# Optimization experiments

Measured on AMD Instinct MI355X. Metric: run time of the kernel, lower is better.

The kernel has to match this reference:

```python
import jax, jax.numpy as jnp
import numpy as np

# pywt db2 decomposition filters
DEC_LO = np.array([-0.12940952255092145, 0.22414386804185735,
                   0.8365163037378079, 0.4829629131445341], dtype=np.float32)
DEC_HI = np.array([-0.4829629131445341, 0.8365163037378079,
                   -0.22414386804185735, -0.12940952255092145], dtype=np.float32)
LEVEL = 3
REC_WEIGHT = 1.0
FILT_LEN = 4
PAD = (2 * FILT_LEN - 3) // 2  # = 2, ptwt reflect padding per side


def _filters(dtype):
    # ptwt uses cross-correlation with flipped pywt filters (== true convolution)
    lo = jnp.asarray(DEC_LO[::-1].copy(), dtype=dtype)
    hi = jnp.asarray(DEC_HI[::-1].copy(), dtype=dtype)
    ll = jnp.outer(lo, lo)  # 'a'
    lh = jnp.outer(hi, lo)  # 'h'
    hl = jnp.outer(lo, hi)  # 'v'
    hh = jnp.outer(hi, hi)  # 'd'
    return jnp.stack([ll, lh, hl, hh])[:, None]  # [4,1,4,4]


def _dwt_step(x, filt):
    # x: [N, nb, H, W] -> [N, 4*nb, H', W'] (each band split into a,h,v,d; grouped)
    n, nb, h, w = x.shape
    padb = PAD + (h % 2)
    padr = PAD + (w % 2)
    xp = jnp.pad(x, ((0, 0), (0, 0), (PAD, padb), (PAD, padr)), mode='reflect')
    k = jnp.tile(filt, (nb, 1, 1, 1))  # [4*nb, 1, 4, 4]
    return jax.lax.conv_general_dilated(
        xp, k, window_strides=(2, 2), padding='VALID',
        feature_group_count=nb,
        dimension_numbers=('NCHW', 'OIHW', 'NCHW'))


def setup_inputs() -> dict:
    key = jax.random.key(0)
    k1, k2 = jax.random.split(key)
    preds = jax.random.normal(k1, (64, 3, 512, 512), dtype=jnp.float32)
    targets = jax.random.normal(k2, (64, 3, 512, 512), dtype=jnp.float32)
    return {"preds": preds, "targets": targets}


def reference(preds, targets):
    n, c, h, w = preds.shape
    p = preds.reshape(n * c, 1, h, w)
    t = targets.reshape(n * c, 1, h, w)
    filt = _filters(preds.dtype)
    for _ in range(LEVEL):
        p = _dwt_step(p, filt)
        t = _dwt_step(t, filt)
    # p, t: [N*C, 4**LEVEL, h', w']; leaf 0 is the all-'a' (pure approx) packet
    per_leaf_mse = jnp.mean((p - t) ** 2, axis=(0, 2, 3))  # [4**LEVEL]
    wvec = jnp.ones(per_leaf_mse.shape[0], dtype=preds.dtype).at[0].set(0.5)
    return REC_WEIGHT * jnp.dot(wvec, per_leaf_mse)
```

## Files before the change

kernel.cpp:

```cpp
#include <hip/hip_runtime.h>

#define F_LO0 0.4829629131445341f
#define F_LO1 0.8365163037378079f
#define F_LO2 0.22414386804185735f
#define F_LO3 (-0.12940952255092145f)
#define F_HI0 (-0.12940952255092145f)
#define F_HI1 (-0.22414386804185735f)
#define F_HI2 0.8365163037378079f
#define F_HI3 (-0.4829629131445341f)

__device__ __forceinline__ int reflect_idx(int r, int n) {
    r = (r < 0) ? -r : r;
    r = (r >= n) ? 2 * n - 2 - r : r;
    return r;
}

__device__ __forceinline__ float4 vfilt(const float4 a, const float4 b,
                                        const float4 c, const float4 d,
                                        float c0, float c1, float c2, float c3) {
    return make_float4(c0 * a.x + c1 * b.x + c2 * c.x + c3 * d.x,
                       c0 * a.y + c1 * b.y + c2 * c.y + c3 * d.y,
                       c0 * a.z + c1 * b.z + c2 * c.z + c3 * d.z,
                       c0 * a.w + c1 * b.w + c2 * c.w + c3 * d.w);
}

__global__ void __launch_bounds__(512) k_wpt_fused(
    const float* __restrict__ p, const float* __restrict__ t,
    float* __restrict__ partial) {
    constexpr int N0 = 512, N1 = 257, N2 = 130, N3 = 66;

    __shared__ __align__(16) float sA[6080];
    __shared__ __align__(16) float sB[6240];
    __shared__ float wsum[8];

    int bid = blockIdx.x;
    int swz = (bid & 7) * (int)(gridDim.x >> 3) + (bid >> 3);
    int img = swz / 81;
    int tt = swz - img * 81;
    int TA = (tt / 9) * 8;
    int TB = (tt % 9) * 8;

    const int tid = threadIdx.x;
    const size_t ibase = (size_t)img * (N0 * N0);

    const int O0r = 8 * TA - 14, O0c = 8 * TB - 16;
    const int O1r = 4 * TA - 6, O1c = 4 * TB - 6;
    const int O2r = 2 * TA - 2, O2c = 2 * TB - 2;
    const bool edge = (TA == 0) || (TA == 64) || (TB == 0) || (TB == 64);

    if (tid < 390) {
        unsigned ru = (unsigned)tid / 5u;
        const int r = (int)ru;
        const int k = tid - (int)(5u * ru);
        const int grr = reflect_idx(O0r + r, N0);
        const float* __restrict__ prow = p + ibase + (size_t)grr * N0;
        const float* __restrict__ trow = t + ibase + (size_t)grr * N0;
        const int gc0 = O0c + 16 * k;
        float v[20];
        if ((unsigned)gc0 <= 492u) {
#pragma unroll
            for (int q = 0; q < 5; ++q) {
                const float4 pv = *(const float4*)(prow + gc0 + 4 * q);
                const float4 tv = *(const float4*)(trow + gc0 + 4 * q);
                v[4 * q + 0] = pv.x - tv.x;
                v[4 * q + 1] = pv.y - tv.y;
                v[4 * q + 2] = pv.z - tv.z;
                v[4 * q + 3] = pv.w - tv.w;
            }
        } else {
#pragma unroll
            for (int x = 0; x < 20; ++x) {
                int gc = reflect_idx(gc0 + x, N0);
                v[x] = prow[gc] - trow[gc];
            }
        }
        float* dst = sB + r * 40 + 8 * k;
        *(float4*)(dst) = make_float4(
            F_LO0 * v[2] + F_LO1 * v[3] + F_LO2 * v[4] + F_LO3 * v[5],
            F_LO0 * v[4] + F_LO1 * v[5] + F_LO2 * v[6] + F_LO3 * v[7],
            F_LO0 * v[6] + F_LO1 * v[7] + F_LO2 * v[8] + F_LO3 * v[9],
            F_LO0 * v[8] + F_LO1 * v[9] + F_LO2 * v[10] + F_LO3 * v[11]);
        *(float4*)(dst + 4) = make_float4(
            F_LO0 * v[10] + F_LO1 * v[11] + F_LO2 * v[12] + F_LO3 * v[13],
            F_LO0 * v[12] + F_LO1 * v[13] + F_LO2 * v[14] + F_LO3 * v[15],
            F_LO0 * v[14] + F_LO1 * v[15] + F_LO2 * v[16] + F_LO3 * v[17],
            F_LO0 * v[16] + F_LO1 * v[17] + F_LO2 * v[18] + F_LO3 * v[19]);
        *(float4*)(dst + 3120) = make_float4(
            F_HI0 * v[2] + F_HI1 * v[3] + F_HI2 * v[4] + F_HI3 * v[5],
            F_HI0 * v[4] + F_HI1 * v[5] + F_HI2 * v[6] + F_HI3 * v[7],
            F_HI0 * v[6] + F_HI1 * v[7] + F_HI2 * v[8] + F_HI3 * v[9],
            F_HI0 * v[8] + F_HI1 * v[9] + F_HI2 * v[10] + F_HI3 * v[11]);
        *(float4*)(dst + 3124) = make_float4(
            F_HI0 * v[10] + F_HI1 * v[11] + F_HI2 * v[12] + F_HI3 * v[13],
            F_HI0 * v[12] + F_HI1 * v[13] + F_HI2 * v[14] + F_HI3 * v[15],
            F_HI0 * v[14] + F_HI1 * v[15] + F_HI2 * v[16] + F_HI3 * v[17],
            F_HI0 * v[16] + F_HI1 * v[17] + F_HI2 * v[18] + F_HI3 * v[19]);
    }
    __syncthreads();

    if (tid < 380) {
        int r1 = tid / 10, k = tid - (tid / 10) * 10;
        const float* blo = sB + (2 * r1) * 40 + 4 * k;
        const float* bhi = blo + 3120;
        float4 L0 = *(const float4*)(blo);
        float4 L1v = *(const float4*)(blo + 40);
        float4 L2v = *(const float4*)(blo + 80);
        float4 L3v = *(const float4*)(blo + 120);
        float4 H0 = *(const float4*)(bhi);
        float4 H1 = *(const float4*)(bhi + 40);
        float4 H2 = *(const float4*)(bhi + 80);
        float4 H3 = *(const float4*)(bhi + 120);
        float4 b0 = vfilt(L0, L1v, L2v, L3v, F_LO0, F_LO1, F_LO2, F_LO3);
        float4 b1 = vfilt(L0, L1v, L2v, L3v, F_HI0, F_HI1, F_HI2, F_HI3);
        float4 b2 = vfilt(H0, H1, H2, H3, F_LO0, F_LO1, F_LO2, F_LO3);
        float4 b3 = vfilt(H0, H1, H2, H3, F_HI0, F_HI1, F_HI2, F_HI3);
        int wo = r1 * 40 + 4 * k;
        *(float4*)(sA + wo) = b0;
        *(float4*)(sA + 1520 + wo) = b1;
        *(float4*)(sA + 3040 + wo) = b2;
        *(float4*)(sA + 4560 + wo) = b3;
    }
    __syncthreads();
    if (edge) {
#pragma unroll
        for (int it = 0; it < 3; ++it) {
            int e = it * 512 + tid;
            if (e < 1444) {
                int lr = e / 38, lc = e - lr * 38;
                int sr = reflect_idx(O1r + lr, N1) - O1r;
                int sc = reflect_idx(O1c + lc, N1) - O1c;
                if ((sr != lr || sc != lc) && (unsigned)sr < 38u && (unsigned)sc < 38u) {
                    int da = lr * 40 + lc;
                    int sa = sr * 40 + sc;
                    sA[da] = sA[sa];
                    sA[1520 + da] = sA[1520 + sa];
                    sA[3040 + da] = sA[3040 + sa];
                    sA[4560 + da] = sA[4560 + sa];
                }
            }
        }
        __syncthreads();
    }

    if (tid < 324) {
        const int r2 = tid / 18, c2 = tid - 18 * r2;
        const int rb = r2 * 80 + 2 * c2;
#pragma unroll
        for (int b = 0; b < 4; ++b) {
            const float* base = sA + b * 1520 + rb;
            float lo[4], hi[4];
#pragma unroll
            for (int u = 0; u < 4; ++u) {
                float2 a = *(const float2*)(base + u * 40);
                float2 d = *(const float2*)(base + u * 40 + 2);
                lo[u] = F_LO0 * a.x + F_LO1 * a.y + F_LO2 * d.x + F_LO3 * d.y;
                hi[u] = F_HI0 * a.x + F_HI1 * a.y + F_HI2 * d.x + F_HI3 * d.y;
            }
            float* dst = sB + (b * 4) * 324 + tid;
            dst[0]       = F_LO0 * lo[0] + F_LO1 * lo[1] + F_LO2 * lo[2] + F_LO3 * lo[3];
            dst[324]     = F_HI0 * lo[0] + F_HI1 * lo[1] + F_HI2 * lo[2] + F_HI3 * lo[3];
            dst[648]     = F_LO0 * hi[0] + F_LO1 * hi[1] + F_LO2 * hi[2] + F_LO3 * hi[3];
            dst[972]     = F_HI0 * hi[0] + F_HI1 * hi[1] + F_HI2 * hi[2] + F_HI3 * hi[3];
        }
    }
    __syncthreads();
    if (edge) {
        if (tid < 324) {
            const int lr = tid / 18, lc = tid - 18 * lr;
            int sr = reflect_idx(O2r + lr, N2) - O2r;
            int sc = reflect_idx(O2c + lc, N2) - O2c;
            if ((sr != lr || sc != lc) && (unsigned)sr < 18u && (unsigned)sc < 18u) {
                int d = lr * 18 + lc;
                int s = sr * 18 + sc;
#pragma unroll
                for (int pl = 0; pl < 16; ++pl) sB[pl * 324 + d] = sB[pl * 324 + s];
            }
        }
        __syncthreads();
    }

    float local = 0.f;
    {
        const int pos = tid & 63;
        const int i = pos >> 3, j = pos & 7;
        const bool valid = (TA + i < N3) && (TB + j < N3);
        const int cell = (2 * i) * 18 + 2 * j;
#pragma unroll
        for (int q = 0; q < 2; ++q) {
            const int pl = (tid >> 6) + 8 * q;
            const float* pb = sB + pl * 324 + cell;
            float lo[4], hi[4];
#pragma unroll
            for (int u = 0; u < 4; ++u) {
                float2 a = *(const float2*)(pb + u * 18);
                float2 d = *(const float2*)(pb + u * 18 + 2);
                lo[u] = F_LO0 * a.x + F_LO1 * a.y + F_LO2 * d.x + F_LO3 * d.y;
                hi[u] = F_HI0 * a.x + F_HI1 * a.y + F_HI2 * d.x + F_HI3 * d.y;
            }
            float o0 = F_LO0 * lo[0] + F_LO1 * lo[1] + F_LO2 * lo[2] + F_LO3 * lo[3];
            float o1 = F_HI0 * lo[0] + F_HI1 * lo[1] + F_HI2 * lo[2] + F_HI3 * lo[3];
            float o2 = F_LO0 * hi[0] + F_LO1 * hi[1] + F_LO2 * hi[2] + F_LO3 * hi[3];
            float o3 = F_HI0 * hi[0] + F_HI1 * hi[1] + F_HI2 * hi[2] + F_HI3 * hi[3];
            if (valid) {
                float w00 = (pl == 0) ? 0.5f : 1.0f;
                local += w00 * o0 * o0 + o1 * o1 + o2 * o2 + o3 * o3;
            }
        }
    }

#pragma unroll
    for (int o = 32; o > 0; o >>= 1) local += __shfl_down(local, o, 64);
    const int w = tid >> 6;
    if ((tid & 63) == 0) wsum[w] = local;
    __syncthreads();
    if (tid == 0) {
        float ssum = 0.f;
#pragma unroll
        for (int x = 0; x < 8; ++x) ssum += wsum[x];
        partial[blockIdx.x] = ssum;
    }
}

__global__ void __launch_bounds__(1024) k_reduce(const float* __restrict__ part,
                                                 float* __restrict__ out,
                                                 int n4, float inv_den) {
    const int tid = threadIdx.x;
    float s = 0.f;
    const float4* p4 = (const float4*)part;
    for (int i = tid; i < n4; i += 1024) {
        float4 v = p4[i];
        s += v.x + v.y + v.z + v.w;
    }
#pragma unroll
    for (int o = 32; o > 0; o >>= 1) s += __shfl_down(s, o, 64);
    __shared__ float ws_[16];
    int w = tid >> 6;
    if ((tid & 63) == 0) ws_[w] = s;
    __syncthreads();
    if (tid == 0) {
        float tot = 0.f;
#pragma unroll
        for (int i = 0; i < 16; ++i) tot += ws_[i];
        out[0] = tot * inv_den;
    }
}

extern "C" void kernel_launch(void* const* d_in, const int* in_sizes, int n_in,
                              void* d_out, int out_size, void* d_ws, size_t ws_size,
                              hipStream_t stream) {
    const float* preds = (const float*)d_in[0];
    const float* targets = (const float*)d_in[1];
    float* out = (float*)d_out;
    float* partial = (float*)d_ws;

    const float inv_den = 1.0f / (192.0f * 66.0f * 66.0f);
    const int nblk = 192 * 9 * 9;

    k_wpt_fused<<<dim3(nblk), dim3(512), 0, stream>>>(preds, targets, partial);
    k_reduce<<<dim3(1), dim3(1024), 0, stream>>>(partial, out, nblk / 4, inv_den);
}
```

Before: 202.3 us.

## Register-block level-2 and level-3 filters to reuse overlapping rows, cap occupancy

```diff
diff --git a/kernel.cpp b/kernel.cpp
--- a/kernel.cpp
+++ b/kernel.cpp
@@ -24,7 +24,7 @@
                        c0 * a.w + c1 * b.w + c2 * c.w + c3 * d.w);
 }
 
-__global__ void __launch_bounds__(512) k_wpt_fused(
+__global__ void __launch_bounds__(512, 6) k_wpt_fused(
     const float* __restrict__ p, const float* __restrict__ t,
     float* __restrict__ partial) {
     constexpr int N0 = 512, N1 = 257, N2 = 130, N3 = 66;
@@ -98,27 +98,32 @@
     }
     __syncthreads();
 
-    if (tid < 380) {
-        int r1 = tid / 10, k = tid - (tid / 10) * 10;
-        const float* blo = sB + (2 * r1) * 40 + 4 * k;
+    if (tid < 190) {
+        const int rp = tid / 10, k = tid - (tid / 10) * 10;
+        const float* blo = sB + (4 * rp) * 40 + 4 * k;
         const float* bhi = blo + 3120;
-        float4 L0 = *(const float4*)(blo);
-        float4 L1v = *(const float4*)(blo + 40);
-        float4 L2v = *(const float4*)(blo + 80);
-        float4 L3v = *(const float4*)(blo + 120);
-        float4 H0 = *(const float4*)(bhi);
-        float4 H1 = *(const float4*)(bhi + 40);
-        float4 H2 = *(const float4*)(bhi + 80);
-        float4 H3 = *(const float4*)(bhi + 120);
-        float4 b0 = vfilt(L0, L1v, L2v, L3v, F_LO0, F_LO1, F_LO2, F_LO3);
-        float4 b1 = vfilt(L0, L1v, L2v, L3v, F_HI0, F_HI1, F_HI2, F_HI3);
-        float4 b2 = vfilt(H0, H1, H2, H3, F_LO0, F_LO1, F_LO2, F_LO3);
-        float4 b3 = vfilt(H0, H1, H2, H3, F_HI0, F_HI1, F_HI2, F_HI3);
-        int wo = r1 * 40 + 4 * k;
-        *(float4*)(sA + wo) = b0;
-        *(float4*)(sA + 1520 + wo) = b1;
-        *(float4*)(sA + 3040 + wo) = b2;
-        *(float4*)(sA + 4560 + wo) = b3;
+        float4 L[6], H[6];
+#pragma unroll
+        for (int j = 0; j < 6; ++j) {
+            L[j] = *(const float4*)(blo + 40 * j);
+            H[j] = *(const float4*)(bhi + 40 * j);
+        }
+#pragma unroll
+        for (int rr = 0; rr < 2; ++rr) {
+            float4 b0 = vfilt(L[2 * rr], L[2 * rr + 1], L[2 * rr + 2], L[2 * rr + 3],
+                              F_LO0, F_LO1, F_LO2, F_LO3);
+            float4 b1 = vfilt(L[2 * rr], L[2 * rr + 1], L[2 * rr + 2], L[2 * rr + 3],
+                              F_HI0, F_HI1, F_HI2, F_HI3);
+            float4 b2 = vfilt(H[2 * rr], H[2 * rr + 1], H[2 * rr + 2], H[2 * rr + 3],
+                              F_LO0, F_LO1, F_LO2, F_LO3);
+            float4 b3 = vfilt(H[2 * rr], H[2 * rr + 1], H[2 * rr + 2], H[2 * rr + 3],
+                              F_HI0, F_HI1, F_HI2, F_HI3);
+            const int wo = (2 * rp + rr) * 40 + 4 * k;
+            *(float4*)(sA + wo) = b0;
+            *(float4*)(sA + 1520 + wo) = b1;
+            *(float4*)(sA + 3040 + wo) = b2;
+            *(float4*)(sA + 4560 + wo) = b3;
+        }
     }
     __syncthreads();
     if (edge) {
@@ -143,7 +148,7 @@
     }
 
     if (tid < 324) {
-        const int r2 = tid / 18, c2 = tid - 18 * r2;
+        const int r2 = tid / 18, c2 = tid - 18 * (tid / 18);
         const int rb = r2 * 80 + 2 * c2;
 #pragma unroll
         for (int b = 0; b < 4; ++b) {
@@ -157,16 +162,16 @@
                 hi[u] = F_HI0 * a.x + F_HI1 * a.y + F_HI2 * d.x + F_HI3 * d.y;
             }
             float* dst = sB + (b * 4) * 324 + tid;
-            dst[0]       = F_LO0 * lo[0] + F_LO1 * lo[1] + F_LO2 * lo[2] + F_LO3 * lo[3];
-            dst[324]     = F_HI0 * lo[0] + F_HI1 * lo[1] + F_HI2 * lo[2] + F_HI3 * lo[3];
-            dst[648]     = F_LO0 * hi[0] + F_LO1 * hi[1] + F_LO2 * hi[2] + F_LO3 * hi[3];
-            dst[972]     = F_HI0 * hi[0] + F_HI1 * hi[1] + F_HI2 * hi[2] + F_HI3 * hi[3];
+            dst[0]   = F_LO0 * lo[0] + F_LO1 * lo[1] + F_LO2 * lo[2] + F_LO3 * lo[3];
+            dst[324] = F_HI0 * lo[0] + F_HI1 * lo[1] + F_HI2 * lo[2] + F_HI3 * lo[3];
+            dst[648] = F_LO0 * hi[0] + F_LO1 * hi[1] + F_LO2 * hi[2] + F_LO3 * hi[3];
+            dst[972] = F_HI0 * hi[0] + F_HI1 * hi[1] + F_HI2 * hi[2] + F_HI3 * hi[3];
         }
     }
     __syncthreads();
     if (edge) {
         if (tid < 324) {
-            const int lr = tid / 18, lc = tid - 18 * lr;
+            const int lr = tid / 18, lc = tid - 18 * (tid / 18);
             int sr = reflect_idx(O2r + lr, N2) - O2r;
             int sc = reflect_idx(O2c + lc, N2) - O2c;
             if ((sr != lr || sc != lc) && (unsigned)sr < 18u && (unsigned)sc < 18u) {
@@ -180,30 +185,38 @@
     }
 
     float local = 0.f;
-    {
-        const int pos = tid & 63;
-        const int i = pos >> 3, j = pos & 7;
-        const bool valid = (TA + i < N3) && (TB + j < N3);
-        const int cell = (2 * i) * 18 + 2 * j;
-#pragma unroll
-        for (int q = 0; q < 2; ++q) {
-            const int pl = (tid >> 6) + 8 * q;
-            const float* pb = sB + pl * 324 + cell;
-            float lo[4], hi[4];
-#pragma unroll
-            for (int u = 0; u < 4; ++u) {
-                float2 a = *(const float2*)(pb + u * 18);
-                float2 d = *(const float2*)(pb + u * 18 + 2);
-                lo[u] = F_LO0 * a.x + F_LO1 * a.y + F_LO2 * d.x + F_LO3 * d.y;
-                hi[u] = F_HI0 * a.x + F_HI1 * a.y + F_HI2 * d.x + F_HI3 * d.y;
-            }
-            float o0 = F_LO0 * lo[0] + F_LO1 * lo[1] + F_LO2 * lo[2] + F_LO3 * lo[3];
-            float o1 = F_HI0 * lo[0] + F_HI1 * lo[1] + F_HI2 * lo[2] + F_HI3 * lo[3];
-            float o2 = F_LO0 * hi[0] + F_LO1 * hi[1] + F_LO2 * hi[2] + F_LO3 * hi[3];
-            float o3 = F_HI0 * hi[0] + F_HI1 * hi[1] + F_HI2 * hi[2] + F_HI3 * hi[3];
-            if (valid) {
-                float w00 = (pl == 0) ? 0.5f : 1.0f;
-                local += w00 * o0 * o0 + o1 * o1 + o2 * o2 + o3 * o3;
+    if (tid < 256) {
+        const int pl = tid >> 4;
+        const int bi = (tid >> 2) & 3, bj = tid & 3;
+        const float* base = sB + pl * 324 + (4 * bi) * 18 + 4 * bj;
+        float hl[6][2], hh[6][2];
+#pragma unroll
+        for (int r = 0; r < 6; ++r) {
+            float2 a = *(const float2*)(base + r * 18);
+            float2 b = *(const float2*)(base + r * 18 + 2);
+            float2 c = *(const float2*)(base + r * 18 + 4);
+            hl[r][0] = F_LO0 * a.x + F_LO1 * a.y + F_LO2 * b.x + F_LO3 * b.y;
+            hl[r][1] = F_LO0 * b.x + F_LO1 * b.y + F_LO2 * c.x + F_LO3 * c.y;
+            hh[r][0] = F_HI0 * a.x + F_HI1 * a.y + F_HI2 * b.x + F_HI3 * b.y;
+            hh[r][1] = F_HI0 * b.x + F_HI1 * b.y + F_HI2 * c.x + F_HI3 * c.y;
+        }
+        const float w00 = (pl == 0) ? 0.5f : 1.0f;
+#pragma unroll
+        for (int du = 0; du < 2; ++du) {
+            const bool rok = (TA + 2 * bi + du < N3);
+#pragma unroll
+            for (int dv = 0; dv < 2; ++dv) {
+                if (rok && (TB + 2 * bj + dv < N3)) {
+                    float o0 = F_LO0 * hl[2 * du][dv] + F_LO1 * hl[2 * du + 1][dv] +
+                               F_LO2 * hl[2 * du + 2][dv] + F_LO3 * hl[2 * du + 3][dv];
+                    float o1 = F_HI0 * hl[2 * du][dv] + F_HI1 * hl[2 * du + 1][dv] +
+                               F_HI2 * hl[2 * du + 2][dv] + F_HI3 * hl[2 * du + 3][dv];
+                    float o2 = F_LO0 * hh[2 * du][dv] + F_LO1 * hh[2 * du + 1][dv] +
+                               F_LO2 * hh[2 * du + 2][dv] + F_LO3 * hh[2 * du + 3][dv];
+                    float o3 = F_HI0 * hh[2 * du][dv] + F_HI1 * hh[2 * du + 1][dv] +
+                               F_HI2 * hh[2 * du + 2][dv] + F_HI3 * hh[2 * du + 3][dv];
+                    local += w00 * o0 * o0 + o1 * o1 + o2 * o2 + o3 * o3;
+                }
             }
         }
     }
```

Measured after the change: 202.5 us. No clear change (+0.1%).
